# Optimization experiments

Hardware: AMD Instinct MI355X
Metric: run time of the kernel (lower is better)

The kernel has to match this reference:

```python
import jax, jax.numpy as jnp
import numpy as np

B, C, T, K = 16, 512, 2048, 64

def setup_inputs() -> dict:
    key = jax.random.key(0)
    k1, k2, k3 = jax.random.split(key, 3)
    v = jax.random.normal(k1, (B, C, T), dtype=jnp.float32)
    # 1x1 Conv1d weights == linear maps over channel dim
    Wk = jax.random.normal(k2, (K, C), dtype=jnp.float32) * 0.02
    bk = jnp.zeros((K,), dtype=jnp.float32)
    Wq = jax.random.normal(k3, (K, C), dtype=jnp.float32) * 0.02
    bq = jnp.zeros((K,), dtype=jnp.float32)
    gamma = jnp.ones((), dtype=jnp.float32)
    return {"v": v, "Wk": Wk, "bk": bk, "Wq": Wq, "bq": bq, "gamma": gamma}

def reference(v, Wk, bk, Wq, bq, gamma):
    # k, q: (B, K, T) via 1x1 conv = channel-wise linear
    k = jnp.einsum('kc,bct->bkt', Wk, v) + bk[None, :, None]
    q = jnp.einsum('kc,bct->bkt', Wq, v) + bq[None, :, None]
    # original: e1[b,d,i,j]=q[b,d,j], e2[b,d,i,j]=k[b,d,i]; sum over d
    # -> s[b,i,j] = sum_d k[b,d,i] * q[b,d,j]  (avoid materializing B,K,T,T)
    s = jnp.einsum('bdi,bdj->bij', k, q)  # (B, T, T)
    a = jax.nn.softmax(s, axis=1)          # softmax over dim=1 (the i axis)
    att = jnp.einsum('bct,btj->bcj', v, a)  # bmm(v, a)
    return v + gamma * att
```

## Files before the change

kernel.cpp:

```cpp
#include <hip/hip_runtime.h>

#define Bc 16
#define Cc 512
#define Tc 2048
#define QT 128
#define KT 64
#define PST 72
#define LTS 66

typedef __attribute__((ext_vector_type(8))) short short8;
typedef __attribute__((ext_vector_type(4))) float f32x4;
typedef unsigned short u16;

static __device__ __forceinline__ u16 f2bf(float x) {
  unsigned u = __float_as_uint(x);
  u += 0x7FFF + ((u >> 16) & 1);
  return (u16)(u >> 16);
}

__global__ __launch_bounds__(256) void prep_kernel(
    const float* __restrict__ Wk, const float* __restrict__ Wq,
    const float* __restrict__ bk, const float* __restrict__ bq,
    u16* __restrict__ Wbf, float* __restrict__ bkq)
{
  int idx  = blockIdx.x * 256 + threadIdx.x;
  int base = idx * 4;
  if (base < 128 * Cc) {
    int ch = base >> 9;
    int c  = base & (Cc - 1);
    const float* src = (ch < 64) ? (Wk + (size_t)ch * Cc + c)
                                 : (Wq + (size_t)(ch - 64) * Cc + c);
    f32x4 w = *reinterpret_cast<const f32x4*>(src);
    uint2 o;
    o.x = (unsigned)f2bf(w[0]) | ((unsigned)f2bf(w[1]) << 16);
    o.y = (unsigned)f2bf(w[2]) | ((unsigned)f2bf(w[3]) << 16);
    *reinterpret_cast<uint2*>(Wbf + base) = o;
  }
  if (idx < 128) bkq[idx] = (idx < 64) ? bk[idx] : bq[idx - 64];
}

__global__ __launch_bounds__(256) void kqv_kernel(
    const float* __restrict__ v, const u16* __restrict__ Wbf,
    const float* __restrict__ bkq, u16* __restrict__ kq, u16* __restrict__ vbf)
{
  __shared__ u16 LDSt[64][LTS];
  const int b   = blockIdx.y;
  const int t0  = blockIdx.x * 64;
  const int tid = threadIdx.x;
  const int lane = tid & 63;
  const int w    = tid >> 6;
  const int l15  = lane & 15;
  const int lg   = lane >> 4;

  f32x4 acc[8];
  #pragma unroll
  for (int mt = 0; mt < 8; ++mt) acc[mt] = f32x4{0.f, 0.f, 0.f, 0.f};

  const float* vb = v + (size_t)b * Cc * Tc + t0;
  float x[16];
  #pragma unroll
  for (int r = 0; r < 16; ++r) x[r] = vb[(size_t)(w * 16 + r) * Tc + lane];

  for (int c0 = 0; c0 < Cc; c0 += 64) {
    __syncthreads();
    #pragma unroll
    for (int r = 0; r < 16; ++r) {
      u16 hb = f2bf(x[r]);
      LDSt[lane][w * 16 + r] = hb;
      vbf[((size_t)b * Cc + c0 + w * 16 + r) * Tc + t0 + lane] = hb;
    }
    __syncthreads();
    if (c0 + 64 < Cc) {
      #pragma unroll
      for (int r = 0; r < 16; ++r)
        x[r] = vb[(size_t)(c0 + 64 + w * 16 + r) * Tc + lane];
    }
    #pragma unroll
    for (int ks = 0; ks < 2; ++ks) {
      short8 bfrag = *reinterpret_cast<const short8*>(&LDSt[w * 16 + l15][ks * 32 + lg * 8]);
      #pragma unroll
      for (int mt = 0; mt < 8; ++mt) {
        short8 afrag = *reinterpret_cast<const short8*>(
            Wbf + (size_t)(mt * 16 + l15) * Cc + c0 + ks * 32 + lg * 8);
        acc[mt] = __builtin_amdgcn_mfma_f32_16x16x32_bf16(afrag, bfrag, acc[mt], 0, 0, 0);
      }
    }
  }
  const int t = t0 + w * 16 + l15;
  u16* op = kq + ((size_t)b * Tc + t) * 128;
  #pragma unroll
  for (int mt = 0; mt < 8; ++mt) {
    int chb = mt * 16 + lg * 4;
    float a0 = acc[mt][0] + bkq[chb + 0];
    float a1 = acc[mt][1] + bkq[chb + 1];
    float a2 = acc[mt][2] + bkq[chb + 2];
    float a3 = acc[mt][3] + bkq[chb + 3];
    uint2 o;
    o.x = (unsigned)f2bf(a0) | ((unsigned)f2bf(a1) << 16);
    o.y = (unsigned)f2bf(a2) | ((unsigned)f2bf(a3) << 16);
    *reinterpret_cast<uint2*>(op + chb) = o;
  }
}

__global__ __launch_bounds__(512, 2) void attn_kernel(
    const float* __restrict__ v, const u16* __restrict__ vbf,
    const u16* __restrict__ kq, const float* __restrict__ gamma_p,
    float* __restrict__ out)
{
  __shared__ u16 P[2][QT * PST];
  __shared__ float scl_lds[2][QT];
  __shared__ float lsum_lds[QT];

  const int L   = blockIdx.x;
  const int lin = (L & 7) * 32 + (L >> 3);
  const int b   = lin >> 4;
  const int j0  = (lin & 15) * QT;
  const int tid = threadIdx.x;
  const int lane = tid & 63;
  const int wid  = tid >> 6;
  const int l15  = lane & 15;
  const int lg   = lane >> 4;
  const int c0   = wid * 64;

  short8 qf0, qf1;
  {
    const u16* qp = kq + (size_t)(b * Tc + j0 + wid * 16 + l15) * 128 + 64 + lg * 8;
    qf0 = *reinterpret_cast<const short8*>(qp);
    qf1 = *reinterpret_cast<const short8*>(qp + 32);
  }

  f32x4 O[4][8];
  #pragma unroll
  for (int a = 0; a < 4; ++a)
    #pragma unroll
    for (int bb = 0; bb < 8; ++bb) O[a][bb] = f32x4{0.f, 0.f, 0.f, 0.f};

  float m = -1e30f, lsum = 0.f;

  const u16* kbase = kq + (size_t)b * Tc * 128 + lg * 8;
  const u16* vbase = vbf + ((size_t)b * Cc + c0) * Tc;

  short8 kf[4][2];
  short8 vf[2][4];
  #pragma unroll
  for (int it = 0; it < 4; ++it) {
    const u16* kp = kbase + (size_t)(it * 16 + l15) * 128;
    kf[it][0] = *reinterpret_cast<const short8*>(kp);
    kf[it][1] = *reinterpret_cast<const short8*>(kp + 32);
  }
  #pragma unroll
  for (int is = 0; is < 2; ++is)
    #pragma unroll
    for (int ct = 0; ct < 4; ++ct)
      vf[is][ct] = *reinterpret_cast<const short8*>(
          vbase + (size_t)(ct * 16 + l15) * Tc + is * 32 + lg * 8);

  int pb = 0;
  for (int i0 = 0; i0 < Tc; i0 += KT, pb ^= 1) {
    f32x4 sacc[4];
    #pragma unroll
    for (int it = 0; it < 4; ++it) {
      f32x4 s = f32x4{0.f, 0.f, 0.f, 0.f};
      s = __builtin_amdgcn_mfma_f32_16x16x32_bf16(kf[it][0], qf0, s, 0, 0, 0);
      s = __builtin_amdgcn_mfma_f32_16x16x32_bf16(kf[it][1], qf1, s, 0, 0, 0);
      sacc[it] = s;
    }
    if (i0 + KT < Tc) {
      #pragma unroll
      for (int it = 0; it < 4; ++it) {
        const u16* kp = kbase + (size_t)(i0 + KT + it * 16 + l15) * 128;
        kf[it][0] = *reinterpret_cast<const short8*>(kp);
        kf[it][1] = *reinterpret_cast<const short8*>(kp + 32);
      }
    }

    float tmax = -1e30f;
    #pragma unroll
    for (int it = 0; it < 4; ++it)
      #pragma unroll
      for (int r = 0; r < 4; ++r) tmax = fmaxf(tmax, sacc[it][r]);
    tmax = fmaxf(tmax, __shfl_xor(tmax, 16));
    tmax = fmaxf(tmax, __shfl_xor(tmax, 32));
    bool defer  = (tmax - m <= 8.f);
    float mnew  = defer ? m : tmax;
    float scale = defer ? 1.f : __expf(m - tmax);
    float psum = 0.f;
    u16 pbv[4][4];
    #pragma unroll
    for (int it = 0; it < 4; ++it)
      #pragma unroll
      for (int r = 0; r < 4; ++r) {
        float p = __expf(sacc[it][r] - mnew);
        psum += p;
        pbv[it][r] = f2bf(p);
      }
    psum += __shfl_xor(psum, 16);
    psum += __shfl_xor(psum, 32);
    lsum = lsum * scale + psum;
    m = mnew;

    {
      u16* prow = &P[pb][(wid * 16 + l15) * PST];
      #pragma unroll
      for (int it = 0; it < 4; ++it) {
        uint2 wv;
        wv.x = (unsigned)pbv[it][0] | ((unsigned)pbv[it][1] << 16);
        wv.y = (unsigned)pbv[it][2] | ((unsigned)pbv[it][3] << 16);
        *reinterpret_cast<uint2*>(prow + it * 16 + lg * 4) = wv;
      }
    }
    if (lane < 16) scl_lds[pb][wid * 16 + lane] = scale;
    __syncthreads();

    float sc[8];
    #pragma unroll
    for (int jj = 0; jj < 8; ++jj) sc[jj] = scl_lds[pb][jj * 16 + l15];
    bool need = false;
    #pragma unroll
    for (int jj = 0; jj < 8; ++jj) need |= (sc[jj] != 1.f);
    if (__any(need)) {
      #pragma unroll
      for (int ct = 0; ct < 4; ++ct)
        #pragma unroll
        for (int jj = 0; jj < 8; ++jj)
          #pragma unroll
          for (int r = 0; r < 4; ++r) O[ct][jj][r] *= sc[jj];
    }

    __builtin_amdgcn_s_setprio(1);
    #pragma unroll
    for (int is = 0; is < 2; ++is) {
      short8 pf[8];
      #pragma unroll
      for (int jj = 0; jj < 8; ++jj)
        pf[jj] = *reinterpret_cast<const short8*>(
            &P[pb][(jj * 16 + l15) * PST + is * 32 + lg * 8]);
      #pragma unroll
      for (int ct = 0; ct < 4; ++ct)
        #pragma unroll
        for (int jj = 0; jj < 8; ++jj)
          O[ct][jj] = __builtin_amdgcn_mfma_f32_16x16x32_bf16(vf[is][ct], pf[jj], O[ct][jj], 0, 0, 0);
    }
    __builtin_amdgcn_s_setprio(0);

    if (i0 + KT < Tc) {
      #pragma unroll
      for (int is = 0; is < 2; ++is)
        #pragma unroll
        for (int ct = 0; ct < 4; ++ct)
          vf[is][ct] = *reinterpret_cast<const short8*>(
              vbase + (size_t)(ct * 16 + l15) * Tc + (i0 + KT) + is * 32 + lg * 8);
    }
  }

  if (lane < 16) lsum_lds[wid * 16 + lane] = lsum;
  __syncthreads();
  const float gamma = *gamma_p;
  #pragma unroll
  for (int jj = 0; jj < 8; ++jj) {
    float linv = gamma / lsum_lds[jj * 16 + l15];
    int j = j0 + jj * 16 + l15;
    #pragma unroll
    for (int ct = 0; ct < 4; ++ct) {
      #pragma unroll
      for (int r = 0; r < 4; ++r) {
        int c = c0 + ct * 16 + lg * 4 + r;
        size_t idx = (size_t)(b * Cc + c) * Tc + j;
        out[idx] = v[idx] + linv * O[ct][jj][r];
      }
    }
  }
}

extern "C" void kernel_launch(void* const* d_in, const int* in_sizes, int n_in,
                              void* d_out, int out_size, void* d_ws, size_t ws_size,
                              hipStream_t stream) {
  const float* v  = (const float*)d_in[0];
  const float* Wk = (const float*)d_in[1];
  const float* bk = (const float*)d_in[2];
  const float* Wq = (const float*)d_in[3];
  const float* bq = (const float*)d_in[4];
  const float* gm = (const float*)d_in[5];
  float* out = (float*)d_out;

  char* ws = (char*)d_ws;
  u16*   kqb = (u16*)ws;
  u16*   vbf = (u16*)(ws + 8388608);
  u16*   Wbf = (u16*)(ws + 8388608 + 33554432);
  float* bkq = (float*)(ws + 8388608 + 33554432 + 131072);

  prep_kernel<<<dim3(64), dim3(256), 0, stream>>>(Wk, Wq, bk, bq, Wbf, bkq);
  kqv_kernel<<<dim3(Tc / 64, Bc), dim3(256), 0, stream>>>(v, Wbf, bkq, kqb, vbf);
  attn_kernel<<<dim3((Tc / QT) * Bc), dim3(512), 0, stream>>>(v, vbf, kqb, gm, out);
}
```

Before: 194.6 us.

## Software-pipeline softmax of next key tile under current PV MFMAs

Restructures the attention loop so the QK scores and softmax for tile i+1 are computed while the PV MFMAs for tile i are issued, with a prologue that handles the first tile and the P/scale double buffer written one stage ahead. The single barrier moves to the end of each iteration. The aim is to overlap exp/max/bf16-conversion VALU work with matrix-core work and hide the softmax latency. In exchange, live register pressure rises (sacc and pw are held across the MFMA block), which at launch bounds of 512 threads with 2 blocks could cause spills.

New measurement: 275.1 us. 41.3% more time.

```diff
diff --git a/kernel.cpp b/kernel.cpp
--- a/kernel.cpp
+++ b/kernel.cpp
@@ -102,6 +102,36 @@
   }
 }
 
+static __device__ __forceinline__ void softmax_tile(
+    const f32x4* sacc, float& m, float& lsum, float& scale, uint2* pw)
+{
+  float tmax = -1e30f;
+  #pragma unroll
+  for (int it = 0; it < 4; ++it)
+    #pragma unroll
+    for (int r = 0; r < 4; ++r) tmax = fmaxf(tmax, sacc[it][r]);
+  tmax = fmaxf(tmax, __shfl_xor(tmax, 16));
+  tmax = fmaxf(tmax, __shfl_xor(tmax, 32));
+  bool defer = (tmax - m <= 8.f);
+  float mnew = defer ? m : tmax;
+  scale = defer ? 1.f : __expf(m - tmax);
+  float psum = 0.f;
+  #pragma unroll
+  for (int it = 0; it < 4; ++it) {
+    float p0 = __expf(sacc[it][0] - mnew);
+    float p1 = __expf(sacc[it][1] - mnew);
+    float p2 = __expf(sacc[it][2] - mnew);
+    float p3 = __expf(sacc[it][3] - mnew);
+    psum += (p0 + p1) + (p2 + p3);
+    pw[it].x = (unsigned)f2bf(p0) | ((unsigned)f2bf(p1) << 16);
+    pw[it].y = (unsigned)f2bf(p2) | ((unsigned)f2bf(p3) << 16);
+  }
+  psum += __shfl_xor(psum, 16);
+  psum += __shfl_xor(psum, 32);
+  lsum = lsum * scale + psum;
+  m = mnew;
+}
+
 __global__ __launch_bounds__(512, 2) void attn_kernel(
     const float* __restrict__ v, const u16* __restrict__ vbf,
     const u16* __restrict__ kq, const float* __restrict__ gamma_p,
@@ -142,21 +172,14 @@
 
   short8 kf[4][2];
   short8 vf[2][4];
+
   #pragma unroll
   for (int it = 0; it < 4; ++it) {
     const u16* kp = kbase + (size_t)(it * 16 + l15) * 128;
     kf[it][0] = *reinterpret_cast<const short8*>(kp);
     kf[it][1] = *reinterpret_cast<const short8*>(kp + 32);
   }
-  #pragma unroll
-  for (int is = 0; is < 2; ++is)
-    #pragma unroll
-    for (int ct = 0; ct < 4; ++ct)
-      vf[is][ct] = *reinterpret_cast<const short8*>(
-          vbase + (size_t)(ct * 16 + l15) * Tc + is * 32 + lg * 8);
-
-  int pb = 0;
-  for (int i0 = 0; i0 < Tc; i0 += KT, pb ^= 1) {
+  {
     f32x4 sacc[4];
     #pragma unroll
     for (int it = 0; it < 4; ++it) {
@@ -165,52 +188,43 @@
       s = __builtin_amdgcn_mfma_f32_16x16x32_bf16(kf[it][1], qf1, s, 0, 0, 0);
       sacc[it] = s;
     }
-    if (i0 + KT < Tc) {
+    float scale;
+    uint2 pw[4];
+    softmax_tile(sacc, m, lsum, scale, pw);
+    u16* prow = &P[0][(wid * 16 + l15) * PST];
+    #pragma unroll
+    for (int it = 0; it < 4; ++it)
+      *reinterpret_cast<uint2*>(prow + it * 16 + lg * 4) = pw[it];
+    if (lane < 16) scl_lds[0][wid * 16 + lane] = scale;
+  }
+  #pragma unroll
+  for (int it = 0; it < 4; ++it) {
+    const u16* kp = kbase + (size_t)(KT + it * 16 + l15) * 128;
+    kf[it][0] = *reinterpret_cast<const short8*>(kp);
+    kf[it][1] = *reinterpret_cast<const short8*>(kp + 32);
+  }
+  #pragma unroll
+  for (int is = 0; is < 2; ++is)
+    #pragma unroll
+    for (int ct = 0; ct < 4; ++ct)
+      vf[is][ct] = *reinterpret_cast<const short8*>(
+          vbase + (size_t)(ct * 16 + l15) * Tc + is * 32 + lg * 8);
+  __syncthreads();
+
+  int pb = 0;
+  for (int i0 = 0; i0 < Tc; i0 += KT, pb ^= 1) {
+    const bool last = (i0 + KT >= Tc);
+
+    f32x4 sacc[4];
+    if (!last) {
       #pragma unroll
       for (int it = 0; it < 4; ++it) {
-        const u16* kp = kbase + (size_t)(i0 + KT + it * 16 + l15) * 128;
-        kf[it][0] = *reinterpret_cast<const short8*>(kp);
-        kf[it][1] = *reinterpret_cast<const short8*>(kp + 32);
+        f32x4 s = f32x4{0.f, 0.f, 0.f, 0.f};
+        s = __builtin_amdgcn_mfma_f32_16x16x32_bf16(kf[it][0], qf0, s, 0, 0, 0);
+        s = __builtin_amdgcn_mfma_f32_16x16x32_bf16(kf[it][1], qf1, s, 0, 0, 0);
+        sacc[it] = s;
       }
     }
-
-    float tmax = -1e30f;
-    #pragma unroll
-    for (int it = 0; it < 4; ++it)
-      #pragma unroll
-      for (int r = 0; r < 4; ++r) tmax = fmaxf(tmax, sacc[it][r]);
-    tmax = fmaxf(tmax, __shfl_xor(tmax, 16));
-    tmax = fmaxf(tmax, __shfl_xor(tmax, 32));
-    bool defer  = (tmax - m <= 8.f);
-    float mnew  = defer ? m : tmax;
-    float scale = defer ? 1.f : __expf(m - tmax);
-    float psum = 0.f;
-    u16 pbv[4][4];
-    #pragma unroll
-    for (int it = 0; it < 4; ++it)
-      #pragma unroll
-      for (int r = 0; r < 4; ++r) {
-        float p = __expf(sacc[it][r] - mnew);
-        psum += p;
-        pbv[it][r] = f2bf(p);
-      }
-    psum += __shfl_xor(psum, 16);
-    psum += __shfl_xor(psum, 32);
-    lsum = lsum * scale + psum;
-    m = mnew;
-
-    {
-      u16* prow = &P[pb][(wid * 16 + l15) * PST];
-      #pragma unroll
-      for (int it = 0; it < 4; ++it) {
-        uint2 wv;
-        wv.x = (unsigned)pbv[it][0] | ((unsigned)pbv[it][1] << 16);
-        wv.y = (unsigned)pbv[it][2] | ((unsigned)pbv[it][3] << 16);
-        *reinterpret_cast<uint2*>(prow + it * 16 + lg * 4) = wv;
-      }
-    }
-    if (lane < 16) scl_lds[pb][wid * 16 + lane] = scale;
-    __syncthreads();
 
     float sc[8];
     #pragma unroll
@@ -227,6 +241,10 @@
           for (int r = 0; r < 4; ++r) O[ct][jj][r] *= sc[jj];
     }
 
+    float scale;
+    uint2 pw[4];
+    if (!last) softmax_tile(sacc, m, lsum, scale, pw);
+
     __builtin_amdgcn_s_setprio(1);
     #pragma unroll
     for (int is = 0; is < 2; ++is) {
@@ -243,13 +261,28 @@
     }
     __builtin_amdgcn_s_setprio(0);
 
-    if (i0 + KT < Tc) {
+    if (!last) {
+      u16* prow = &P[pb ^ 1][(wid * 16 + l15) * PST];
+      #pragma unroll
+      for (int it = 0; it < 4; ++it)
+        *reinterpret_cast<uint2*>(prow + it * 16 + lg * 4) = pw[it];
+      if (lane < 16) scl_lds[pb ^ 1][wid * 16 + lane] = scale;
+
+      if (i0 + 2 * KT < Tc) {
+        #pragma unroll
+        for (int it = 0; it < 4; ++it) {
+          const u16* kp = kbase + (size_t)(i0 + 2 * KT + it * 16 + l15) * 128;
+          kf[it][0] = *reinterpret_cast<const short8*>(kp);
+          kf[it][1] = *reinterpret_cast<const short8*>(kp + 32);
+        }
+      }
       #pragma unroll
       for (int is = 0; is < 2; ++is)
         #pragma unroll
         for (int ct = 0; ct < 4; ++ct)
           vf[is][ct] = *reinterpret_cast<const short8*>(
               vbase + (size_t)(ct * 16 + l15) * Tc + (i0 + KT) + is * 32 + lg * 8);
+      __syncthreads();
     }
   }
 
```
